# Optimization experiments

Hardware: AMD Instinct MI355X
Metric: run time of the kernel (lower is better)

Reference implementation:

```python
import jax, jax.numpy as jnp
import numpy as np

N_NODES = 100000
N_EDGES = 3200000
D_IN = 128
D_OUT = 128


def setup_inputs() -> dict:
    key = jax.random.key(0)
    k1, k2, k3, k4, k5 = jax.random.split(key, 5)
    x = jax.random.normal(k1, (N_NODES, D_IN), dtype=jnp.float32)
    edge_row = jnp.sort(jax.random.randint(k2, (N_EDGES,), 0, N_NODES))
    edge_col = jax.random.randint(k3, (N_EDGES,), 0, N_NODES)
    edge_val = jax.random.uniform(k4, (N_EDGES,), dtype=jnp.float32)
    W = jax.random.normal(k5, (D_IN, D_OUT), dtype=jnp.float32) * (1.0 / np.sqrt(D_IN))
    return {"x": x, "edge_row": edge_row, "edge_col": edge_col,
            "edge_val": edge_val, "W": W}


def reference(x, edge_row, edge_col, edge_val, W):
    # h = spmm(adj_norm, x): gather source features, scale by edge weight,
    # scatter-add into destination rows.
    msgs = edge_val[:, None] * x[edge_col]            # [E, D_IN]
    h = jax.ops.segment_sum(msgs, edge_row, num_segments=N_NODES)  # [N, D_IN]
    # dense linear projection (no bias)
    return h @ W                                       # [N, D_OUT]
```

## Files before the change

### kernel.cpp

```cpp
#include <hip/hip_runtime.h>
#include <hip/hip_bf16.h>

#define D 128
#define D2U 64

typedef __attribute__((ext_vector_type(8))) short  short8;
typedef __attribute__((ext_vector_type(4))) float  f32x4;
typedef __attribute__((ext_vector_type(2))) float  f32x2;

__device__ __forceinline__ unsigned f2bf(float f) {
    unsigned u = __float_as_uint(f);
    u += 0x7FFFu + ((u >> 16) & 1u);
    return u >> 16;
}
__device__ __forceinline__ unsigned pk2(float a, float b) {
    return f2bf(a) | (f2bf(b) << 16);
}
__device__ __forceinline__ float bflo(unsigned u) { return __uint_as_float(u << 16); }
__device__ __forceinline__ float bfhi(unsigned u) { return __uint_as_float(u & 0xFFFF0000u); }

__global__ __launch_bounds__(256, 2) void gemm_mfma_kernel(
    const float* __restrict__ x, const float* __restrict__ W,
    unsigned* __restrict__ y, int n_nodes, int ntiles)
{
    __shared__ unsigned short Wt[D * D];

    const int t = threadIdx.x;

    {
        const float4* W4 = reinterpret_cast<const float4*>(W);
#pragma unroll
        for (int m = 0; m < 16; ++m) {
            const int idx4 = m * 256 + t;
            const int k  = idx4 >> 5;
            const int c0 = (idx4 & 31) << 2;
            const float4 w = W4[idx4];
            const float wv[4] = {w.x, w.y, w.z, w.w};
#pragma unroll
            for (int i = 0; i < 4; ++i) {
                const int c    = c0 + i;
                const int slot = (k >> 3) ^ (c & 15);
                Wt[c * 128 + slot * 8 + (k & 7)] = (unsigned short)f2bf(wv[i]);
            }
        }
    }
    __syncthreads();

    const int lane = t & 63;
    const int cl   = lane & 15;
    const int g    = lane >> 4;

    short8 wf[8][4];
#pragma unroll
    for (int ct = 0; ct < 8; ++ct)
#pragma unroll
        for (int ks = 0; ks < 4; ++ks) {
            const int c    = ct * 16 + cl;
            const int slot = (ks * 4 + g) ^ cl;
            wf[ct][ks] = *reinterpret_cast<const short8*>(&Wt[c * 128 + slot * 8]);
        }

    const int wave   = (blockIdx.x << 2) | (t >> 6);
    const int nwaves = gridDim.x << 2;

#define LOADX(rt_, buf_)                                                      \
    {                                                                         \
        int r_ = (rt_) * 16 + cl;                                             \
        if (r_ >= n_nodes) r_ = n_nodes - 1;                                  \
        const float* p_ = x + (size_t)r_ * D + g * 8;                         \
        _Pragma("unroll")                                                     \
        for (int ks_ = 0; ks_ < 4; ++ks_) {                                   \
            buf_[2 * ks_]     = *reinterpret_cast<const float4*>(p_ + ks_ * 32);     \
            buf_[2 * ks_ + 1] = *reinterpret_cast<const float4*>(p_ + ks_ * 32 + 4); \
        }                                                                     \
    }

#define COMPUTE(rt_, buf_)                                                    \
    {                                                                         \
        f32x4 acc_[8];                                                        \
        _Pragma("unroll")                                                     \
        for (int ct_ = 0; ct_ < 8; ++ct_) acc_[ct_] = (f32x4)(0.f);           \
        _Pragma("unroll")                                                     \
        for (int ks_ = 0; ks_ < 4; ++ks_) {                                   \
            short8 xf_;                                                       \
            unsigned* xu_ = reinterpret_cast<unsigned*>(&xf_);                \
            const float4 a_ = buf_[2 * ks_], b_ = buf_[2 * ks_ + 1];          \
            xu_[0] = pk2(a_.x, a_.y); xu_[1] = pk2(a_.z, a_.w);               \
            xu_[2] = pk2(b_.x, b_.y); xu_[3] = pk2(b_.z, b_.w);               \
            _Pragma("unroll")                                                 \
            for (int ct_ = 0; ct_ < 8; ++ct_)                                 \
                acc_[ct_] = __builtin_amdgcn_mfma_f32_16x16x32_bf16(          \
                    wf[ct_][ks_], xf_, acc_[ct_], 0, 0, 0);                   \
        }                                                                     \
        const int r_ = (rt_) * 16 + cl;                                       \
        if (r_ < n_nodes) {                                                   \
            unsigned* yp_ = y + (size_t)r_ * D2U + g * 2;                     \
            _Pragma("unroll")                                                 \
            for (int ct_ = 0; ct_ < 8; ++ct_) {                               \
                uint2 v2_ = make_uint2(pk2(acc_[ct_][0], acc_[ct_][1]),       \
                                       pk2(acc_[ct_][2], acc_[ct_][3]));      \
                *reinterpret_cast<uint2*>(yp_ + ct_ * 8) = v2_;               \
            }                                                                 \
        }                                                                     \
    }

    int rt = wave;
    if (rt >= ntiles) return;
    float4 bufA[8], bufB[8];
    LOADX(rt, bufA);
    while (true) {
        int nxt = rt + nwaves;
        if (nxt < ntiles) {
            LOADX(nxt, bufB);
            COMPUTE(rt, bufA);
            rt = nxt;
            nxt = rt + nwaves;
            if (nxt < ntiles) {
                LOADX(nxt, bufA);
                COMPUTE(rt, bufB);
                rt = nxt;
            } else { COMPUTE(rt, bufB); break; }
        } else { COMPUTE(rt, bufA); break; }
    }
#undef LOADX
#undef COMPUTE
}

__global__ __launch_bounds__(256) void build_rowptr_kernel(
    const int* __restrict__ row, int* __restrict__ ptr, int n_edges, int n_nodes)
{
    int e = blockIdx.x * blockDim.x + threadIdx.x;
    if (e > n_edges) return;
    int lo, hi;
    if (e == 0)            { lo = -1;               hi = row[0];   }
    else if (e == n_edges) { lo = row[n_edges - 1]; hi = n_nodes;  }
    else {
        lo = row[e - 1];
        hi = row[e];
        if (lo == hi) return;
    }
    for (int r = lo + 1; r <= hi; ++r) ptr[r] = e;
}

#define EUNR 8

__global__ __launch_bounds__(256) void spmm_kernel(
    const unsigned* __restrict__ yb, const int* __restrict__ ptr,
    const int* __restrict__ col, const float* __restrict__ val,
    float2* __restrict__ out2, int n_nodes)
{
    int gid  = blockIdx.x * blockDim.x + threadIdx.x;
    int r    = gid >> 6;
    int lane = threadIdx.x & 63;
    if (r >= n_nodes) return;

    const int s = ptr[r];
    const int e = ptr[r + 1];

    float ax = 0.f, ay = 0.f;
    const int nb = (e - s) >> 3;
    int i = s + (nb << 3);

    int      cA[EUNR], cB[EUNR];
    float    vA[EUNR], vB[EUNR];
    unsigned uA[EUNR], uB[EUNR];

#define ISSUE(tb_, C_, V_, U_)                                     \
    {                                                              \
        const int base_ = s + ((tb_) << 3);                        \
        _Pragma("unroll")                                          \
        for (int k_ = 0; k_ < EUNR; ++k_) {                        \
            C_[k_] = col[base_ + k_];                              \
            V_[k_] = val[base_ + k_];                              \
        }                                                          \
        _Pragma("unroll")                                          \
        for (int k_ = 0; k_ < EUNR; ++k_)                          \
            U_[k_] = yb[(size_t)C_[k_] * D2U + lane];              \
    }
#define CONSUME(V_, U_)                                            \
    {                                                              \
        _Pragma("unroll")                                          \
        for (int k_ = 0; k_ < EUNR; ++k_) {                        \
            ax += V_[k_] * bflo(U_[k_]);                           \
            ay += V_[k_] * bfhi(U_[k_]);                           \
        }                                                          \
    }

    if (nb > 0) {
        ISSUE(0, cA, vA, uA);
        int tb = 0;
        while (tb + 1 < nb) {
            ISSUE(tb + 1, cB, vB, uB);
            CONSUME(vA, uA);
            ++tb;
            if (tb + 1 < nb) {
                ISSUE(tb + 1, cA, vA, uA);
                CONSUME(vB, uB);
                ++tb;
            } else {
                CONSUME(vB, uB);
                ++tb;
            }
        }
        if (tb < nb) CONSUME(vA, uA);
    }
#undef ISSUE
#undef CONSUME

    for (; i + 4 <= e; i += 4) {
        const int   c0 = col[i],     c1 = col[i + 1], c2 = col[i + 2], c3 = col[i + 3];
        const float v0 = val[i],     v1 = val[i + 1], v2 = val[i + 2], v3 = val[i + 3];
        const unsigned u0 = yb[(size_t)c0 * D2U + lane];
        const unsigned u1 = yb[(size_t)c1 * D2U + lane];
        const unsigned u2 = yb[(size_t)c2 * D2U + lane];
        const unsigned u3 = yb[(size_t)c3 * D2U + lane];
        ax += v0 * bflo(u0); ay += v0 * bfhi(u0);
        ax += v1 * bflo(u1); ay += v1 * bfhi(u1);
        ax += v2 * bflo(u2); ay += v2 * bfhi(u2);
        ax += v3 * bflo(u3); ay += v3 * bfhi(u3);
    }
    for (; i < e; ++i) {
        const int      c = col[i];
        const float    v = val[i];
        const unsigned u = yb[(size_t)c * D2U + lane];
        ax += v * bflo(u); ay += v * bfhi(u);
    }

    f32x2 o;
    o.x = ax; o.y = ay;
    __builtin_nontemporal_store(o,
        reinterpret_cast<f32x2*>(out2 + (size_t)r * D2U + lane));
}

extern "C" void kernel_launch(void* const* d_in, const int* in_sizes, int n_in,
                              void* d_out, int out_size, void* d_ws, size_t ws_size,
                              hipStream_t stream)
{
    const float* x        = (const float*)d_in[0];
    const int*   edge_row = (const int*)  d_in[1];
    const int*   edge_col = (const int*)  d_in[2];
    const float* edge_val = (const float*)d_in[3];
    const float* W        = (const float*)d_in[4];
    float*       out      = (float*)d_out;

    const int n_nodes = in_sizes[0] / D;
    const int n_edges = in_sizes[1];
    const int ntiles  = (n_nodes + 15) / 16;

    unsigned* y   = (unsigned*)d_ws;
    int*      ptr = (int*)((char*)d_ws + (size_t)n_nodes * D2U * sizeof(unsigned));

    gemm_mfma_kernel<<<512, 256, 0, stream>>>(x, W, y, n_nodes, ntiles);

    {
        int blocks = (n_edges + 1 + 255) / 256;
        build_rowptr_kernel<<<blocks, 256, 0, stream>>>(edge_row, ptr, n_edges, n_nodes);
    }
    {
        int rows_per_block = 256 / 64;
        int blocks = (n_nodes + rows_per_block - 1) / rows_per_block;
        spmm_kernel<<<blocks, 256, 0, stream>>>(y, ptr, edge_col, edge_val,
                                                (float2*)out, n_nodes);
    }
}
```

Before: 163.4 us.

## Restructure SpMM row loop into padded three-stage software pipeline with scalar row bounds

Row bounds are read with readfirstlane so the edge index and value loads can become wave-uniform scalar loads. The tail loops are gone: every row is processed in padded blocks of eight, with out-of-range slots clamped to the last edge and given a zero weight. The loop becomes a three-stage pipeline in which index loads run two blocks ahead and feature gathers one block ahead of the accumulation, aiming to hide gather latency better. In exchange, short rows now issue wasted padded gathers and more registers are held live.

```diff
diff --git a/kernel.cpp b/kernel.cpp
--- a/kernel.cpp
+++ b/kernel.cpp
@@ -142,8 +142,6 @@
     for (int r = lo + 1; r <= hi; ++r) ptr[r] = e;
 }
 
-#define EUNR 8
-
 __global__ __launch_bounds__(256) void spmm_kernel(
     const unsigned* __restrict__ yb, const int* __restrict__ ptr,
     const int* __restrict__ col, const float* __restrict__ val,
@@ -154,77 +152,65 @@
     int lane = threadIdx.x & 63;
     if (r >= n_nodes) return;
 
-    const int s = ptr[r];
-    const int e = ptr[r + 1];
+    const int s = __builtin_amdgcn_readfirstlane(ptr[r]);
+    const int e = __builtin_amdgcn_readfirstlane(ptr[r + 1]);
+    const int nb = (e - s + 7) >> 3;
 
     float ax = 0.f, ay = 0.f;
-    const int nb = (e - s) >> 3;
-    int i = s + (nb << 3);
-
-    int      cA[EUNR], cB[EUNR];
-    float    vA[EUNR], vB[EUNR];
-    unsigned uA[EUNR], uB[EUNR];
-
-#define ISSUE(tb_, C_, V_, U_)                                     \
-    {                                                              \
-        const int base_ = s + ((tb_) << 3);                        \
-        _Pragma("unroll")                                          \
-        for (int k_ = 0; k_ < EUNR; ++k_) {                        \
-            C_[k_] = col[base_ + k_];                              \
-            V_[k_] = val[base_ + k_];                              \
-        }                                                          \
-        _Pragma("unroll")                                          \
-        for (int k_ = 0; k_ < EUNR; ++k_)                          \
-            U_[k_] = yb[(size_t)C_[k_] * D2U + lane];              \
-    }
-#define CONSUME(V_, U_)                                            \
-    {                                                              \
-        _Pragma("unroll")                                          \
-        for (int k_ = 0; k_ < EUNR; ++k_) {                        \
-            ax += V_[k_] * bflo(U_[k_]);                           \
-            ay += V_[k_] * bfhi(U_[k_]);                           \
-        }                                                          \
+
+#define SLOAD(bk_, C_, V_)                                           \
+    {                                                                \
+        const int base_ = s + ((bk_) << 3);                          \
+        _Pragma("unroll")                                            \
+        for (int k_ = 0; k_ < 8; ++k_) {                             \
+            const int idx_ = base_ + k_;                             \
+            const int si_  = (idx_ < e) ? idx_ : (e - 1);            \
+            C_[k_] = col[si_];                                       \
+            const float vv_ = val[si_];                              \
+            V_[k_] = (idx_ < e) ? vv_ : 0.f;                         \
+        }                                                            \
+    }
+#define GATHER(C_, U_)                                               \
+    {                                                                \
+        _Pragma("unroll")                                            \
+        for (int k_ = 0; k_ < 8; ++k_)                               \
+            U_[k_] = yb[((size_t)C_[k_] << 6) + lane];               \
+    }
+#define CONSUME(U_, V_)                                              \
+    {                                                                \
+        _Pragma("unroll")                                            \
+        for (int k_ = 0; k_ < 8; ++k_) {                             \
+            ax += V_[k_] * bflo(U_[k_]);                             \
+            ay += V_[k_] * bfhi(U_[k_]);                             \
+        }                                                            \
     }
 
     if (nb > 0) {
-        ISSUE(0, cA, vA, uA);
-        int tb = 0;
-        while (tb + 1 < nb) {
-            ISSUE(tb + 1, cB, vB, uB);
-            CONSUME(vA, uA);
-            ++tb;
-            if (tb + 1 < nb) {
-                ISSUE(tb + 1, cA, vA, uA);
-                CONSUME(vB, uB);
-                ++tb;
-            } else {
-                CONSUME(vB, uB);
-                ++tb;
-            }
+        int      c0[8], c1[8];
+        float    v0[8], v1[8];
+        unsigned uA[8], uB[8];
+
+        SLOAD(0, c0, v0);
+        GATHER(c0, uA);
+        if (nb > 1) SLOAD(1, c1, v1);
+
+        int bk = 0;
+        while (true) {
+            if (bk + 1 < nb) GATHER(c1, uB);
+            CONSUME(uA, v0);
+            if (bk + 2 < nb) SLOAD(bk + 2, c0, v0);
+            ++bk;
+            if (bk >= nb) break;
+            if (bk + 1 < nb) GATHER(c0, uA);
+            CONSUME(uB, v1);
+            if (bk + 2 < nb) SLOAD(bk + 2, c1, v1);
+            ++bk;
+            if (bk >= nb) break;
         }
-        if (tb < nb) CONSUME(vA, uA);
-    }
-#undef ISSUE
+    }
+#undef SLOAD
+#undef GATHER
 #undef CONSUME
-
-    for (; i + 4 <= e; i += 4) {
-        const int   c0 = col[i],     c1 = col[i + 1], c2 = col[i + 2], c3 = col[i + 3];
-        const float v0 = val[i],     v1 = val[i + 1], v2 = val[i + 2], v3 = val[i + 3];
-        const unsigned u0 = yb[(size_t)c0 * D2U + lane];
-        const unsigned u1 = yb[(size_t)c1 * D2U + lane];
-        const unsigned u2 = yb[(size_t)c2 * D2U + lane];
-        const unsigned u3 = yb[(size_t)c3 * D2U + lane];
-        ax += v0 * bflo(u0); ay += v0 * bfhi(u0);
-        ax += v1 * bflo(u1); ay += v1 * bfhi(u1);
-        ax += v2 * bflo(u2); ay += v2 * bfhi(u2);
-        ax += v3 * bflo(u3); ay += v3 * bfhi(u3);
-    }
-    for (; i < e; ++i) {
-        const int      c = col[i];
-        const float    v = val[i];
-        const unsigned u = yb[(size_t)c * D2U + lane];
-        ax += v * bflo(u); ay += v * bfhi(u);
-    }
 
     f32x2 o;
     o.x = ax; o.y = ay;
```

Result: slower. 181.5 us (+11.1%).

## Restructure SpMM edge loop to prefetch indices with 16-wide gather batches

Applied to the files above, without the earlier changes.

Replaces the double-buffered 8-edge gather pipeline with a loop that issues 16 feature-row gathers at once and prefetches the next batch of column indices and values while accumulating. Row pointers are made wave-uniform via readfirstlane so index and value loads can go through scalar paths. This aims to raise memory-level parallelism and cut address and branch overhead. In exchange it uses more registers, and rows with fewer than 16 edges (average degree is 32) fall through to the 4-wide tail loop more often.

```diff
diff --git a/kernel.cpp b/kernel.cpp
--- a/kernel.cpp
+++ b/kernel.cpp
@@ -142,7 +142,7 @@
     for (int r = lo + 1; r <= hi; ++r) ptr[r] = e;
 }
 
-#define EUNR 8
+#define EUNR 16
 
 __global__ __launch_bounds__(256) void spmm_kernel(
     const unsigned* __restrict__ yb, const int* __restrict__ ptr,
@@ -154,58 +154,46 @@
     int lane = threadIdx.x & 63;
     if (r >= n_nodes) return;
 
-    const int s = ptr[r];
-    const int e = ptr[r + 1];
+    const int s = __builtin_amdgcn_readfirstlane(ptr[r]);
+    const int e = __builtin_amdgcn_readfirstlane(ptr[r + 1]);
 
     float ax = 0.f, ay = 0.f;
-    const int nb = (e - s) >> 3;
-    int i = s + (nb << 3);
-
-    int      cA[EUNR], cB[EUNR];
-    float    vA[EUNR], vB[EUNR];
-    unsigned uA[EUNR], uB[EUNR];
-
-#define ISSUE(tb_, C_, V_, U_)                                     \
-    {                                                              \
-        const int base_ = s + ((tb_) << 3);                        \
-        _Pragma("unroll")                                          \
-        for (int k_ = 0; k_ < EUNR; ++k_) {                        \
-            C_[k_] = col[base_ + k_];                              \
-            V_[k_] = val[base_ + k_];                              \
-        }                                                          \
-        _Pragma("unroll")                                          \
-        for (int k_ = 0; k_ < EUNR; ++k_)                          \
-            U_[k_] = yb[(size_t)C_[k_] * D2U + lane];              \
-    }
-#define CONSUME(V_, U_)                                            \
-    {                                                              \
-        _Pragma("unroll")                                          \
-        for (int k_ = 0; k_ < EUNR; ++k_) {                        \
-            ax += V_[k_] * bflo(U_[k_]);                           \
-            ay += V_[k_] * bfhi(U_[k_]);                           \
-        }                                                          \
-    }
-
-    if (nb > 0) {
-        ISSUE(0, cA, vA, uA);
-        int tb = 0;
-        while (tb + 1 < nb) {
-            ISSUE(tb + 1, cB, vB, uB);
-            CONSUME(vA, uA);
-            ++tb;
-            if (tb + 1 < nb) {
-                ISSUE(tb + 1, cA, vA, uA);
-                CONSUME(vB, uB);
-                ++tb;
-            } else {
-                CONSUME(vB, uB);
-                ++tb;
+    int i = s;
+
+    if (i + EUNR <= e) {
+        int   c[EUNR];
+        float v[EUNR];
+#pragma unroll
+        for (int k = 0; k < EUNR; ++k) { c[k] = col[i + k]; v[k] = val[i + k]; }
+
+        while (true) {
+            unsigned u[EUNR];
+#pragma unroll
+            for (int k = 0; k < EUNR; ++k)
+                u[k] = yb[(size_t)c[k] * D2U + lane];
+
+            const int  ni   = i + EUNR;
+            const bool more = (ni + EUNR <= e);
+
+            int   nc[EUNR];
+            float nv[EUNR];
+            if (more) {
+#pragma unroll
+                for (int k = 0; k < EUNR; ++k) { nc[k] = col[ni + k]; nv[k] = val[ni + k]; }
             }
+
+#pragma unroll
+            for (int k = 0; k < EUNR; ++k) {
+                ax += v[k] * bflo(u[k]);
+                ay += v[k] * bfhi(u[k]);
+            }
+
+            i = ni;
+            if (!more) break;
+#pragma unroll
+            for (int k = 0; k < EUNR; ++k) { c[k] = nc[k]; v[k] = nv[k]; }
         }
-        if (tb < nb) CONSUME(vA, uA);
-    }
-#undef ISSUE
-#undef CONSUME
+    }
 
     for (; i + 4 <= e; i += 4) {
         const int   c0 = col[i],     c1 = col[i + 1], c2 = col[i + 2], c3 = col[i + 3];
```

Measured after the change: 143.5 us. 1.14x faster.
